# Kernel tuning notes

Measured on AMD Instinct MI355X. Metric: run time of the kernel, lower is better.

Reference implementation:

```python
import jax, jax.numpy as jnp
import numpy as np

B, D, M = 64, 256, 100  # batch, reduced channel dim, h*w of feature map (10x10)

# Precompute upper-triangle (including diagonal) flat indices for Triuvec
_r, _c = np.triu_indices(D)
FLAT_TRIU_IDX = jnp.asarray(_r * D + _c)  # [D*(D+1)/2]


def setup_inputs() -> dict:
    key = jax.random.key(0)
    k1, = jax.random.split(key, 1)
    feat_map = jax.random.normal(k1, (B, D, M), dtype=jnp.float32)
    # temperature param init: log(1 / (2 * h * w)) with h = w = 10
    temperature = jnp.full((1, 1), np.log(1.0 / (2 * 10 * 10)), dtype=jnp.float32)
    return {"feat_map": feat_map, "temperature": temperature}


def reference(feat_map, temperature):
    # feat_map: [B, D, M]; temperature: [1, 1] learned scalar
    b, d, m = feat_map.shape
    f1 = feat_map[:, :, None, :]  # [B, D, 1, M]
    f2 = feat_map[:, None, :, :]  # [B, 1, D, M]
    # item_1 - item_2, summed over map dim; idea_variant path: (i1 - i2)/2 * exp(T)
    out = 0.5 * jnp.sum(jnp.abs(f1 + f2) - jnp.abs(f1 - f2), axis=-1)  # [B, D, D]
    out = out * jnp.exp(temperature[0, 0])
    # normalize_bdc double-centering: out - (1/D) out @ 1 - (1/D) 1 @ out
    row = jnp.sum(out, axis=2, keepdims=True) / d  # [B, D, 1]
    col = jnp.sum(out, axis=1, keepdims=True) / d  # [B, 1, D]
    out = out - row - col
    # Triuvec (with diagonal): gather upper-triangle entries
    vec = out.reshape(b, d * d)[:, FLAT_TRIU_IDX]  # [B, D*(D+1)/2]
    return vec
```

## Files before the change

kernel.cpp:

```cpp
#include <hip/hip_runtime.h>


#define NB 64
#define DD 256
#define MM 100
#define TILE 64
#define NUT 10
#define TRI_PER_B 32896
#define NTILE 640
#define NM2 50
#define TILE_F (TILE * TILE)

typedef unsigned int u32;
typedef _Float16 f16x2 __attribute__((ext_vector_type(2)));
typedef _Float16 f16x4 __attribute__((ext_vector_type(4)));

__device__ __forceinline__ void tile_coords(int t, int& ti, int& tj) {
    int a = (t >= 4) + (t >= 7) + (t >= 9);
    int s = (a * (9 - a)) >> 1;
    ti = a;
    tj = t - s + a;
}

__device__ __forceinline__ u32 slot_enc(int g) {
    return g == 0 ? 0x03020100u : g == 1 ? 0x21060504u
         : g == 2 ? 0x25220807u : 0x28262309u;
}

__device__ __forceinline__ int swz_bt(int w) { return (w & 7) * 80 + (w >> 3); }

extern "C" __global__ void __launch_bounds__(256, 4)
k_partial(const float* __restrict__ f, float* __restrict__ part,
          _Float16* __restrict__ tiles) {
    __shared__ u32 As[NM2][TILE];
    __shared__ u32 Bs[NM2][TILE];
    const int t = threadIdx.x;
    const int bt = swz_bt(blockIdx.x);
    const int b = bt / NUT;
    const int ut = bt % NUT;
    int ti, tj;
    tile_coords(ut, ti, tj);
    const int i0 = ti * TILE, j0 = tj * TILE;
    const float* fb = f + (size_t)b * DD * MM;

    for (int l = t; l < TILE * 25; l += 256) {
        const int il = l & 63;
        const int mq = l >> 6;
        float4 v = *reinterpret_cast<const float4*>(fb + (size_t)(i0 + il) * MM + mq * 4);
        As[2 * mq + 0][il] = __builtin_bit_cast(u32, __builtin_amdgcn_cvt_pkrtz(v.x, v.y));
        As[2 * mq + 1][il] = __builtin_bit_cast(u32, __builtin_amdgcn_cvt_pkrtz(v.z, v.w));
        float4 w = *reinterpret_cast<const float4*>(fb + (size_t)(j0 + il) * MM + mq * 4);
        Bs[2 * mq + 0][il] = __builtin_bit_cast(u32, __builtin_amdgcn_cvt_pkrtz(w.x, w.y));
        Bs[2 * mq + 1][il] = __builtin_bit_cast(u32, __builtin_amdgcn_cvt_pkrtz(w.z, w.w));
    }
    __syncthreads();

    const int tix = t & 15, tiy = t >> 4;
    float acc[4][4] = {};

    #pragma unroll 5
    for (int m2 = 0; m2 < NM2; ++m2) {
        uint4 afu = *reinterpret_cast<const uint4*>(&As[m2][tix * 4]);
        uint4 bfu = *reinterpret_cast<const uint4*>(&Bs[m2][tiy * 4]);
        const u32 av[4] = {afu.x, afu.y, afu.z, afu.w};
        const u32 bv[4] = {bfu.x, bfu.y, bfu.z, bfu.w};
        u32 aab[4], aso[4], bab[4], bsg[4];
        #pragma unroll
        for (int q = 0; q < 4; ++q) {
            aab[q] = av[q] & 0x7fff7fffu;
            aso[q] = (av[q] & 0x80008000u) | 0x3c003c00u;
        }
        #pragma unroll
        for (int r = 0; r < 4; ++r) {
            bab[r] = bv[r] & 0x7fff7fffu;
            bsg[r] = bv[r] & 0x80008000u;
        }
        #pragma unroll
        for (int q = 0; q < 4; ++q) {
            #pragma unroll
            for (int r = 0; r < 4; ++r) {
                u32 so = aso[q] ^ bsg[r];
                f16x2 mn = __builtin_elementwise_min(
                    __builtin_bit_cast(f16x2, aab[q]),
                    __builtin_bit_cast(f16x2, bab[r]));
                acc[q][r] = __builtin_amdgcn_fdot2(
                    mn, __builtin_bit_cast(f16x2, so), acc[q][r], false);
            }
        }
    }

    _Float16* tp = tiles + (size_t)bt * TILE_F;
    #pragma unroll
    for (int q = 0; q < 4; ++q) {
        f16x4 hv;
        hv.x = (_Float16)acc[q][0]; hv.y = (_Float16)acc[q][1];
        hv.z = (_Float16)acc[q][2]; hv.w = (_Float16)acc[q][3];
        *reinterpret_cast<f16x4*>(tp + (tix * 4 + q) * TILE + tiy * 4) = hv;
    }

    float ra[4], cb[4];
    #pragma unroll
    for (int q = 0; q < 4; ++q)
        ra[q] = (acc[q][0] + acc[q][1]) + (acc[q][2] + acc[q][3]);
    #pragma unroll
    for (int r = 0; r < 4; ++r)
        cb[r] = (acc[0][r] + acc[1][r]) + (acc[2][r] + acc[3][r]);

    __syncthreads();
    float* red  = reinterpret_cast<float*>(&As[0][0]);
    float* red2 = reinterpret_cast<float*>(&Bs[0][0]);
    #pragma unroll
    for (int q = 0; q < 4; ++q) red[tiy * 64 + tix * 4 + q] = ra[q];
    #pragma unroll
    for (int r = 0; r < 4; ++r) red2[tix * 64 + tiy * 4 + r] = cb[r];
    __syncthreads();

    const size_t pbase = (size_t)bt * 128;
    if (t < TILE) {
        float s = 0.f;
        #pragma unroll
        for (int w = 0; w < 16; ++w) s += red[w * 64 + t];
        part[pbase + t] = s;
    } else if (t < 2 * TILE && ti != tj) {
        const int u = t - TILE;
        float s = 0.f;
        #pragma unroll
        for (int w = 0; w < 16; ++w) s += red2[w * 64 + u];
        part[pbase + 64 + u] = s;
    }
}

extern "C" __global__ void __launch_bounds__(256)
k_finalize(const float* __restrict__ part, const float* __restrict__ temp,
           const _Float16* __restrict__ tiles, float* __restrict__ out) {
    __shared__ float rows_sh[128];
    const int t = threadIdx.x;
    const int bt = swz_bt(blockIdx.x);
    const int b = bt / NUT;
    const int ut = bt % NUT;
    int ti, tj;
    tile_coords(ut, ti, tj);
    const int i0 = ti * TILE, j0 = tj * TILE;
    const int tix = t >> 4, tiy = t & 15;

    if (t < 128) {
        const int half = t >> 6, u = t & 63;
        const int g = half ? tj : ti;
        const u32 enc = slot_enc(g);
        float sum = 0.f;
        #pragma unroll
        for (int s = 0; s < 4; ++s) {
            const u32 byte = (enc >> (8 * s)) & 0xffu;
            const int ut_s = byte & 0x1f;
            const int side = byte >> 5;
            sum += part[(size_t)(b * NUT + ut_s) * 128 + side * 64 + u];
        }
        rows_sh[t] = sum;
    }

    const _Float16* tp = tiles + (size_t)bt * TILE_F;
    float acc[4][4];
    #pragma unroll
    for (int q = 0; q < 4; ++q) {
        f16x4 v = *reinterpret_cast<const f16x4*>(tp + (tix * 4 + q) * TILE + tiy * 4);
        acc[q][0] = (float)v.x; acc[q][1] = (float)v.y;
        acc[q][2] = (float)v.z; acc[q][3] = (float)v.w;
    }
    __syncthreads();

    const float scale = expf(temp[0]);
    const float inv_d = 1.0f / DD;
    const int cbase = (ti == tj) ? 0 : 64;
    float rloc[4], cloc[4];
    #pragma unroll
    for (int q = 0; q < 4; ++q) rloc[q] = rows_sh[tix * 4 + q];
    #pragma unroll
    for (int r = 0; r < 4; ++r) cloc[r] = rows_sh[cbase + tiy * 4 + r];

    float* ob = out + (size_t)b * TRI_PER_B;
    #pragma unroll
    for (int q = 0; q < 4; ++q) {
        const int i = i0 + tix * 4 + q;
        float v[4];
        #pragma unroll
        for (int r = 0; r < 4; ++r)
            v[r] = scale * (acc[q][r] - (rloc[q] + cloc[r]) * inv_d);
        const int j0e = j0 + tiy * 4;
        if (ti != tj) {
            const int off = (i * (2 * DD - i + 1)) / 2 + (j0e - i);
            *reinterpret_cast<float4*>(ob + off) = make_float4(v[0], v[1], v[2], v[3]);
        } else {
            #pragma unroll
            for (int r = 0; r < 4; ++r) {
                const int j = j0e + r;
                if (j >= i) {
                    const int off = (i * (2 * DD - i + 1)) / 2 + (j - i);
                    ob[off] = v[r];
                }
            }
        }
    }
}

extern "C" void kernel_launch(void* const* d_in, const int* in_sizes, int n_in,
                              void* d_out, int out_size, void* d_ws, size_t ws_size,
                              hipStream_t stream) {
    const float* f    = (const float*)d_in[0];
    const float* temp = (const float*)d_in[1];
    float* out  = (float*)d_out;
    float* part = (float*)d_ws;
    _Float16* tiles = (_Float16*)(part + NTILE * 128);

    k_partial<<<NTILE, 256, 0, stream>>>(f, part, tiles);
    k_finalize<<<NTILE, 256, 0, stream>>>(part, temp, tiles, out);
}
```

Before: 35.14 us.

## Fuse partial and finalize kernels via per-batch atomic barrier

Merges the two kernels into one. Each block keeps its fp16 tile in shared memory instead of writing it to global, then waits on a per-batch atomic counter until all 10 tiles of that batch have published their row and column partial sums, and applies the centering and triangular store directly. This removes the second launch and the global tile round trip. In exchange it adds a memset launch and a spin-wait that relies on all 10 blocks of a batch being co-resident, which the grid size and swizzle are expected to guarantee.

```diff
diff --git a/kernel.cpp b/kernel.cpp
--- a/kernel.cpp
+++ b/kernel.cpp
@@ -9,11 +9,9 @@
 #define TRI_PER_B 32896
 #define NTILE 640
 #define NM2 50
-#define TILE_F (TILE * TILE)
 
 typedef unsigned int u32;
 typedef _Float16 f16x2 __attribute__((ext_vector_type(2)));
-typedef _Float16 f16x4 __attribute__((ext_vector_type(4)));
 
 __device__ __forceinline__ void tile_coords(int t, int& ti, int& tj) {
     int a = (t >= 4) + (t >= 7) + (t >= 9);
@@ -30,8 +28,9 @@
 __device__ __forceinline__ int swz_bt(int w) { return (w & 7) * 80 + (w >> 3); }
 
 extern "C" __global__ void __launch_bounds__(256, 4)
-k_partial(const float* __restrict__ f, float* __restrict__ part,
-          _Float16* __restrict__ tiles) {
+k_fused(const float* __restrict__ f, const float* __restrict__ temp,
+        float* __restrict__ part, u32* __restrict__ ctr,
+        float* __restrict__ out) {
     __shared__ u32 As[NM2][TILE];
     __shared__ u32 Bs[NM2][TILE];
     const int t = threadIdx.x;
@@ -89,15 +88,6 @@
         }
     }
 
-    _Float16* tp = tiles + (size_t)bt * TILE_F;
-    #pragma unroll
-    for (int q = 0; q < 4; ++q) {
-        f16x4 hv;
-        hv.x = (_Float16)acc[q][0]; hv.y = (_Float16)acc[q][1];
-        hv.z = (_Float16)acc[q][2]; hv.w = (_Float16)acc[q][3];
-        *reinterpret_cast<f16x4*>(tp + (tix * 4 + q) * TILE + tiy * 4) = hv;
-    }
-
     float ra[4], cb[4];
     #pragma unroll
     for (int q = 0; q < 4; ++q)
@@ -107,12 +97,20 @@
         cb[r] = (acc[0][r] + acc[1][r]) + (acc[2][r] + acc[3][r]);
 
     __syncthreads();
-    float* red  = reinterpret_cast<float*>(&As[0][0]);
-    float* red2 = reinterpret_cast<float*>(&Bs[0][0]);
+    float* red   = reinterpret_cast<float*>(&As[0][0]);
+    float* red2  = red + 1024;
+    u32*   stash = &Bs[0][0];
     #pragma unroll
     for (int q = 0; q < 4; ++q) red[tiy * 64 + tix * 4 + q] = ra[q];
     #pragma unroll
     for (int r = 0; r < 4; ++r) red2[tix * 64 + tiy * 4 + r] = cb[r];
+    #pragma unroll
+    for (int q = 0; q < 4; ++q) {
+        stash[(2 * q + 0) * 256 + t] =
+            __builtin_bit_cast(u32, __builtin_amdgcn_cvt_pkrtz(acc[q][0], acc[q][1]));
+        stash[(2 * q + 1) * 256 + t] =
+            __builtin_bit_cast(u32, __builtin_amdgcn_cvt_pkrtz(acc[q][2], acc[q][3]));
+    }
     __syncthreads();
 
     const size_t pbase = (size_t)bt * 128;
@@ -128,21 +126,21 @@
         for (int w = 0; w < 16; ++w) s += red2[w * 64 + u];
         part[pbase + 64 + u] = s;
     }
-}
-
-extern "C" __global__ void __launch_bounds__(256)
-k_finalize(const float* __restrict__ part, const float* __restrict__ temp,
-           const _Float16* __restrict__ tiles, float* __restrict__ out) {
-    __shared__ float rows_sh[128];
-    const int t = threadIdx.x;
-    const int bt = swz_bt(blockIdx.x);
-    const int b = bt / NUT;
-    const int ut = bt % NUT;
-    int ti, tj;
-    tile_coords(ut, ti, tj);
-    const int i0 = ti * TILE, j0 = tj * TILE;
-    const int tix = t >> 4, tiy = t & 15;
-
+    __syncthreads();
+
+    if (t == 0) {
+        __threadfence();
+        atomicAdd(&ctr[b], 1u);
+        while (atomicAdd(&ctr[b], 0u) < NUT)
+            __builtin_amdgcn_s_sleep(2);
+        __threadfence();
+    }
+    __syncthreads();
+
+    const int ftix = t >> 4, ftiy = t & 15;
+    const int to = ((t & 15) << 4) | (t >> 4);
+
+    float* rows_sh = red;
     if (t < 128) {
         const int half = t >> 6, u = t & 63;
         const int g = half ? tj : ti;
@@ -157,35 +155,35 @@
         }
         rows_sh[t] = sum;
     }
-
-    const _Float16* tp = tiles + (size_t)bt * TILE_F;
-    float acc[4][4];
+    __syncthreads();
+
+    float vv[4][4];
     #pragma unroll
     for (int q = 0; q < 4; ++q) {
-        f16x4 v = *reinterpret_cast<const f16x4*>(tp + (tix * 4 + q) * TILE + tiy * 4);
-        acc[q][0] = (float)v.x; acc[q][1] = (float)v.y;
-        acc[q][2] = (float)v.z; acc[q][3] = (float)v.w;
-    }
-    __syncthreads();
+        f16x2 w0 = __builtin_bit_cast(f16x2, stash[(2 * q + 0) * 256 + to]);
+        f16x2 w1 = __builtin_bit_cast(f16x2, stash[(2 * q + 1) * 256 + to]);
+        vv[q][0] = (float)w0.x; vv[q][1] = (float)w0.y;
+        vv[q][2] = (float)w1.x; vv[q][3] = (float)w1.y;
+    }
 
     const float scale = expf(temp[0]);
     const float inv_d = 1.0f / DD;
     const int cbase = (ti == tj) ? 0 : 64;
     float rloc[4], cloc[4];
     #pragma unroll
-    for (int q = 0; q < 4; ++q) rloc[q] = rows_sh[tix * 4 + q];
-    #pragma unroll
-    for (int r = 0; r < 4; ++r) cloc[r] = rows_sh[cbase + tiy * 4 + r];
+    for (int q = 0; q < 4; ++q) rloc[q] = rows_sh[ftix * 4 + q];
+    #pragma unroll
+    for (int r = 0; r < 4; ++r) cloc[r] = rows_sh[cbase + ftiy * 4 + r];
 
     float* ob = out + (size_t)b * TRI_PER_B;
     #pragma unroll
     for (int q = 0; q < 4; ++q) {
-        const int i = i0 + tix * 4 + q;
+        const int i = i0 + ftix * 4 + q;
         float v[4];
         #pragma unroll
         for (int r = 0; r < 4; ++r)
-            v[r] = scale * (acc[q][r] - (rloc[q] + cloc[r]) * inv_d);
-        const int j0e = j0 + tiy * 4;
+            v[r] = scale * (vv[q][r] - (rloc[q] + cloc[r]) * inv_d);
+        const int j0e = j0 + ftiy * 4;
         if (ti != tj) {
             const int off = (i * (2 * DD - i + 1)) / 2 + (j0e - i);
             *reinterpret_cast<float4*>(ob + off) = make_float4(v[0], v[1], v[2], v[3]);
@@ -209,8 +207,8 @@
     const float* temp = (const float*)d_in[1];
     float* out  = (float*)d_out;
     float* part = (float*)d_ws;
-    _Float16* tiles = (_Float16*)(part + NTILE * 128);
-
-    k_partial<<<NTILE, 256, 0, stream>>>(f, part, tiles);
-    k_finalize<<<NTILE, 256, 0, stream>>>(part, temp, tiles, out);
-}
+    u32* ctr = (u32*)(part + NTILE * 128);
+
+    hipMemsetAsync(ctr, 0, NB * sizeof(u32), stream);
+    k_fused<<<NTILE, 256, 0, stream>>>(f, temp, part, ctr, out);
+}
```

New measurement: 64.20 us. 1.83x slower.

## Split each pairwise tile into two half-width column blocks with register prefetch

Applied to the files above, without the earlier changes.

The partial kernel now launches twice as many blocks, and each one computes a 64x32 half tile instead of 64x64. Each thread holds a 4x2 accumulator and prefetches the next shared-memory row into registers. The partial-sum layout grows to 192 floats per tile, so the two halves' row sums are stored separately and combined in the finalize kernel. The aim is more parallelism and occupancy (launch bounds raised to 5 blocks per SM) for a grid that was small, at the cost of loading the A tile twice and making more, smaller blocks.

```diff
diff --git a/kernel.cpp b/kernel.cpp
--- a/kernel.cpp
+++ b/kernel.cpp
@@ -10,6 +10,7 @@
 #define NTILE 640
 #define NM2 50
 #define TILE_F (TILE * TILE)
+#define PSTRIDE 192
 
 typedef unsigned int u32;
 typedef _Float16 f16x2 __attribute__((ext_vector_type(2)));
@@ -29,18 +30,21 @@
 
 __device__ __forceinline__ int swz_bt(int w) { return (w & 7) * 80 + (w >> 3); }
 
-extern "C" __global__ void __launch_bounds__(256, 4)
+extern "C" __global__ void __launch_bounds__(256, 5)
 k_partial(const float* __restrict__ f, float* __restrict__ part,
           _Float16* __restrict__ tiles) {
     __shared__ u32 As[NM2][TILE];
-    __shared__ u32 Bs[NM2][TILE];
+    __shared__ u32 Bs[NM2][32];
     const int t = threadIdx.x;
-    const int bt = swz_bt(blockIdx.x);
+    const int unit = (blockIdx.x & 7) * 160 + (blockIdx.x >> 3);
+    const int bt = unit >> 1;
+    const int half = unit & 1;
     const int b = bt / NUT;
     const int ut = bt % NUT;
     int ti, tj;
     tile_coords(ut, ti, tj);
-    const int i0 = ti * TILE, j0 = tj * TILE;
+    const int i0 = ti * TILE;
+    const int j0 = tj * TILE + half * 32;
     const float* fb = f + (size_t)b * DD * MM;
 
     for (int l = t; l < TILE * 25; l += 256) {
@@ -49,84 +53,93 @@
         float4 v = *reinterpret_cast<const float4*>(fb + (size_t)(i0 + il) * MM + mq * 4);
         As[2 * mq + 0][il] = __builtin_bit_cast(u32, __builtin_amdgcn_cvt_pkrtz(v.x, v.y));
         As[2 * mq + 1][il] = __builtin_bit_cast(u32, __builtin_amdgcn_cvt_pkrtz(v.z, v.w));
+    }
+    for (int l = t; l < 32 * 25; l += 256) {
+        const int il = l & 31;
+        const int mq = l >> 5;
         float4 w = *reinterpret_cast<const float4*>(fb + (size_t)(j0 + il) * MM + mq * 4);
         Bs[2 * mq + 0][il] = __builtin_bit_cast(u32, __builtin_amdgcn_cvt_pkrtz(w.x, w.y));
         Bs[2 * mq + 1][il] = __builtin_bit_cast(u32, __builtin_amdgcn_cvt_pkrtz(w.z, w.w));
     }
     __syncthreads();
 
-    const int tix = t & 15, tiy = t >> 4;
-    float acc[4][4] = {};
-
+    const int cg = t & 15;
+    const int rg = t >> 4;
+    float acc[4][2] = {};
+
+    uint4 af = *reinterpret_cast<const uint4*>(&As[0][rg * 4]);
+    uint2 bf = *reinterpret_cast<const uint2*>(&Bs[0][cg * 2]);
     #pragma unroll 5
     for (int m2 = 0; m2 < NM2; ++m2) {
-        uint4 afu = *reinterpret_cast<const uint4*>(&As[m2][tix * 4]);
-        uint4 bfu = *reinterpret_cast<const uint4*>(&Bs[m2][tiy * 4]);
-        const u32 av[4] = {afu.x, afu.y, afu.z, afu.w};
-        const u32 bv[4] = {bfu.x, bfu.y, bfu.z, bfu.w};
-        u32 aab[4], aso[4], bab[4], bsg[4];
+        uint4 an;
+        uint2 bn;
+        if (m2 + 1 < NM2) {
+            an = *reinterpret_cast<const uint4*>(&As[m2 + 1][rg * 4]);
+            bn = *reinterpret_cast<const uint2*>(&Bs[m2 + 1][cg * 2]);
+        }
+        const u32 av[4] = {af.x, af.y, af.z, af.w};
+        const u32 bv[2] = {bf.x, bf.y};
+        u32 aab[4], aso[4], bab[2], bsg[2];
         #pragma unroll
         for (int q = 0; q < 4; ++q) {
             aab[q] = av[q] & 0x7fff7fffu;
             aso[q] = (av[q] & 0x80008000u) | 0x3c003c00u;
         }
         #pragma unroll
-        for (int r = 0; r < 4; ++r) {
-            bab[r] = bv[r] & 0x7fff7fffu;
-            bsg[r] = bv[r] & 0x80008000u;
+        for (int c = 0; c < 2; ++c) {
+            bab[c] = bv[c] & 0x7fff7fffu;
+            bsg[c] = bv[c] & 0x80008000u;
         }
         #pragma unroll
         for (int q = 0; q < 4; ++q) {
             #pragma unroll
-            for (int r = 0; r < 4; ++r) {
-                u32 so = aso[q] ^ bsg[r];
+            for (int c = 0; c < 2; ++c) {
+                u32 so = aso[q] ^ bsg[c];
                 f16x2 mn = __builtin_elementwise_min(
                     __builtin_bit_cast(f16x2, aab[q]),
-                    __builtin_bit_cast(f16x2, bab[r]));
-                acc[q][r] = __builtin_amdgcn_fdot2(
-                    mn, __builtin_bit_cast(f16x2, so), acc[q][r], false);
+                    __builtin_bit_cast(f16x2, bab[c]));
+                acc[q][c] = __builtin_amdgcn_fdot2(
+                    mn, __builtin_bit_cast(f16x2, so), acc[q][c], false);
             }
         }
+        af = an; bf = bn;
     }
 
     _Float16* tp = tiles + (size_t)bt * TILE_F;
     #pragma unroll
     for (int q = 0; q < 4; ++q) {
-        f16x4 hv;
-        hv.x = (_Float16)acc[q][0]; hv.y = (_Float16)acc[q][1];
-        hv.z = (_Float16)acc[q][2]; hv.w = (_Float16)acc[q][3];
-        *reinterpret_cast<f16x4*>(tp + (tix * 4 + q) * TILE + tiy * 4) = hv;
-    }
-
-    float ra[4], cb[4];
-    #pragma unroll
-    for (int q = 0; q < 4; ++q)
-        ra[q] = (acc[q][0] + acc[q][1]) + (acc[q][2] + acc[q][3]);
-    #pragma unroll
-    for (int r = 0; r < 4; ++r)
-        cb[r] = (acc[0][r] + acc[1][r]) + (acc[2][r] + acc[3][r]);
+        *reinterpret_cast<u32*>(tp + (rg * 4 + q) * TILE + half * 32 + cg * 2) =
+            __builtin_bit_cast(u32, __builtin_amdgcn_cvt_pkrtz(acc[q][0], acc[q][1]));
+    }
+
+    float ra[4], cb[2];
+    #pragma unroll
+    for (int q = 0; q < 4; ++q) ra[q] = acc[q][0] + acc[q][1];
+    #pragma unroll
+    for (int c = 0; c < 2; ++c)
+        cb[c] = (acc[0][c] + acc[1][c]) + (acc[2][c] + acc[3][c]);
 
     __syncthreads();
     float* red  = reinterpret_cast<float*>(&As[0][0]);
-    float* red2 = reinterpret_cast<float*>(&Bs[0][0]);
-    #pragma unroll
-    for (int q = 0; q < 4; ++q) red[tiy * 64 + tix * 4 + q] = ra[q];
-    #pragma unroll
-    for (int r = 0; r < 4; ++r) red2[tix * 64 + tiy * 4 + r] = cb[r];
-    __syncthreads();
-
-    const size_t pbase = (size_t)bt * 128;
+    float* red2 = red + 1024;
+    #pragma unroll
+    for (int q = 0; q < 4; ++q) red[cg * 64 + rg * 4 + q] = ra[q];
+    #pragma unroll
+    for (int c = 0; c < 2; ++c) red2[rg * 32 + cg * 2 + c] = cb[c];
+    __syncthreads();
+
+    float* pb = part + (size_t)bt * PSTRIDE;
     if (t < TILE) {
         float s = 0.f;
         #pragma unroll
         for (int w = 0; w < 16; ++w) s += red[w * 64 + t];
-        part[pbase + t] = s;
-    } else if (t < 2 * TILE && ti != tj) {
+        pb[half * 64 + t] = s;
+    } else if (t < TILE + 32 && ti != tj) {
         const int u = t - TILE;
         float s = 0.f;
         #pragma unroll
-        for (int w = 0; w < 16; ++w) s += red2[w * 64 + u];
-        part[pbase + 64 + u] = s;
+        for (int w = 0; w < 16; ++w) s += red2[w * 32 + u];
+        pb[128 + half * 32 + u] = s;
     }
 }
 
@@ -144,8 +157,8 @@
     const int tix = t >> 4, tiy = t & 15;
 
     if (t < 128) {
-        const int half = t >> 6, u = t & 63;
-        const int g = half ? tj : ti;
+        const int hr = t >> 6, u = t & 63;
+        const int g = hr ? tj : ti;
         const u32 enc = slot_enc(g);
         float sum = 0.f;
         #pragma unroll
@@ -153,7 +166,8 @@
             const u32 byte = (enc >> (8 * s)) & 0xffu;
             const int ut_s = byte & 0x1f;
             const int side = byte >> 5;
-            sum += part[(size_t)(b * NUT + ut_s) * 128 + side * 64 + u];
+            const float* pb = part + (size_t)(b * NUT + ut_s) * PSTRIDE;
+            sum += side ? pb[128 + u] : (pb[u] + pb[64 + u]);
         }
         rows_sh[t] = sum;
     }
@@ -209,8 +223,8 @@
     const float* temp = (const float*)d_in[1];
     float* out  = (float*)d_out;
     float* part = (float*)d_ws;
-    _Float16* tiles = (_Float16*)(part + NTILE * 128);
-
-    k_partial<<<NTILE, 256, 0, stream>>>(f, part, tiles);
+    _Float16* tiles = (_Float16*)(part + NTILE * PSTRIDE);
+
+    k_partial<<<2 * NTILE, 256, 0, stream>>>(f, part, tiles);
     k_finalize<<<NTILE, 256, 0, stream>>>(part, temp, tiles, out);
 }
```

Measured after the change: 36.17 us. 2.9% more time.
